# Optimization experiments

Measured on AMD Instinct MI355X. Metric: run time of the kernel, lower is better.

Reference implementation:

```python
import jax, jax.numpy as jnp
import numpy as np

DIM = 1024
HEADS = 8
HEAD_DIM = DIM // HEADS
TAU = HEAD_DIM ** 0.5
BS, SEQ = 1, 2048


def setup_inputs() -> dict:
    key = jax.random.key(0)
    kq, kk, kv, kb = jax.random.split(key, 4)
    q = jax.random.normal(kq, (BS, SEQ, DIM), jnp.float32)
    k = jax.random.normal(kk, (BS, SEQ, DIM), jnp.float32)
    v = jax.random.normal(kv, (BS, SEQ, DIM), jnp.float32)
    Wi_w = jnp.zeros((HEADS, 3 * DIM), jnp.float32)
    Wi_b = 0.1 * jax.random.normal(kb, (HEADS,), jnp.float32)
    Wf_w = jnp.zeros((HEADS, 3 * DIM), jnp.float32)
    Wf_b = jnp.linspace(3.0, 6.0, HEADS, dtype=jnp.float32)  # equidistant_bias_init(3, 6)
    gn_w = jnp.ones((DIM,), jnp.float32)
    gn_b = jnp.zeros((DIM,), jnp.float32)
    return {"q": q, "k": k, "v": v, "Wi_w": Wi_w, "Wi_b": Wi_b,
            "Wf_w": Wf_w, "Wf_b": Wf_b, "gn_w": gn_w, "gn_b": gn_b}


def reference(q, k, v, Wi_w, Wi_b, Wf_w, Wf_b, gn_w, gn_b):
    bs, seq, dim = q.shape
    gate_in = jnp.concatenate([q, k, v], axis=-1)                    # [b, s, 3d]
    itilde = jnp.einsum('bsd,hd->bhs', gate_in, Wi_w) + Wi_b[None, :, None]
    ftilde = jnp.einsum('bsd,hd->bhs', gate_in, Wf_w) + Wf_b[None, :, None]

    # Decay matrix: F_act[i,j] = sum_{t=j+1..i} logsigmoid(ftilde_t), lower-tri else -inf
    csum = jnp.cumsum(jax.nn.log_sigmoid(ftilde), axis=-1)           # [b, h, s]
    Fmat = csum[..., :, None] - csum[..., None, :]                   # [b, h, s, s]
    mask = jnp.tril(jnp.ones((seq, seq), dtype=bool))
    F_act = jnp.where(mask, Fmat, -jnp.inf)

    Dtilde = F_act + itilde[..., None, :]                            # add input gate along j
    max_d = jnp.max(Dtilde, axis=-1, keepdims=True)
    D = jnp.exp(Dtilde - max_d)                                      # stabilized decay weights

    qh = q.reshape(bs, seq, HEADS, HEAD_DIM).transpose(0, 2, 1, 3)
    kh = k.reshape(bs, seq, HEADS, HEAD_DIM).transpose(0, 2, 1, 3)
    vh = v.reshape(bs, seq, HEADS, HEAD_DIM).transpose(0, 2, 1, 3)

    Ctilde = jnp.einsum('bhid,bhjd->bhij', qh, kh) * D / TAU
    maxit = jnp.maximum(jnp.abs(jnp.sum(Ctilde, axis=-1, keepdims=True)), jnp.exp(-max_d))
    Htilde = jnp.einsum('bhij,bhjd->bhid', Ctilde, vh) / (maxit + 1e-6)

    # GroupNorm(HEADS groups) over dim, applied per token
    x = Htilde.transpose(0, 2, 1, 3).reshape(bs * seq, HEADS, HEAD_DIM)
    mean = jnp.mean(x, axis=-1, keepdims=True)
    var = jnp.var(x, axis=-1, keepdims=True)
    xn = (x - mean) / jnp.sqrt(var + 1e-5)
    out = xn.reshape(bs * seq, DIM) * gn_w + gn_b
    return out.reshape(bs, seq, DIM)
```

## Files before the change

### kernel.cpp

```cpp
#include <hip/hip_runtime.h>
#include <math.h>

#define SEQ 2048
#define NH 8
#define HD 128
#define DIMF 1024
#define LOG2E 1.4426950408889634f
#define INVTAU 0.08838834764831845f

typedef __attribute__((ext_vector_type(8))) short bf16x8;
typedef __attribute__((ext_vector_type(8))) unsigned short us8;
typedef __attribute__((ext_vector_type(4))) float f32x4;

__device__ float g_itacc[NH*SEQ];
__device__ float g_ftacc[NH*SEQ];
__device__ float g_aL[NH*SEQ];
__device__ float g_cmL[NH*SEQ];
__device__ float g_en[NH*SEQ];
__device__ unsigned short g_Qb[NH*SEQ*HD];
__device__ unsigned short g_Kb[NH*SEQ*HD];
__device__ unsigned short g_Vb[NH*SEQ*HD];
__device__ unsigned short g_Vt[NH*HD*SEQ];
__device__ unsigned short g_Wb[16*3072];

__device__ __forceinline__ unsigned short f2bf(float x) {
  unsigned u = __float_as_uint(x);
  u += 0x7fffu + ((u >> 16) & 1u);
  return (unsigned short)(u >> 16);
}

__global__ __launch_bounds__(256) void convert_kernel(const float* __restrict__ q,
                                                      const float* __restrict__ k,
                                                      const float* __restrict__ v,
                                                      const float* __restrict__ Wi,
                                                      const float* __restrict__ Wf) {
  const int bid = blockIdx.x;
  if (bid < 6144) {
    const int s = bid & 2047;
    const int t = bid >> 11;
    const float* src = (t == 0) ? q : (t == 1) ? k : v;
    unsigned short* dst = (t == 0) ? g_Qb : (t == 1) ? g_Kb : g_Vb;
    const int c = threadIdx.x * 4;
    const float4 f = *(const float4*)(src + s*DIMF + c);
    const int h = c >> 7, d = c & 127;
    ushort4 u;
    u.x = f2bf(f.x); u.y = f2bf(f.y); u.z = f2bf(f.z); u.w = f2bf(f.w);
    *(ushort4*)(dst + (h*SEQ + s)*HD + d) = u;
  } else {
    const int gid = (bid - 6144) * 256 + threadIdx.x;
    const int e4 = gid * 4;
    const int p = e4 / 3072;
    const int c = e4 % 3072;
    const float* src = (p < 8) ? (Wi + p*3072 + c) : (Wf + (p-8)*3072 + c);
    const float4 f = *(const float4*)src;
    ushort4 u;
    u.x = f2bf(f.x); u.y = f2bf(f.y); u.z = f2bf(f.z); u.w = f2bf(f.w);
    *(ushort4*)(g_Wb + p*3072 + c) = u;
  }
}

__global__ __launch_bounds__(256) void vtrans_kernel() {
  __shared__ __align__(16) unsigned short Ts[64*72];
  const int h  = blockIdx.x;
  const int s0 = blockIdx.y * 64;
  const int d0 = blockIdx.z * 64;
  const int t = threadIdx.x;
  {
    const int sr = t >> 2;
    const int c  = (t & 3) * 16;
    const unsigned short* src = g_Vb + (h*SEQ + s0 + sr)*HD + d0 + c;
    *(us8*)&Ts[sr*72 + c]     = *(const us8*)&src[0];
    *(us8*)&Ts[sr*72 + c + 8] = *(const us8*)&src[8];
  }
  __syncthreads();
  {
    const int w = t >> 6, l = t & 63;
    unsigned short outv[16];
    #pragma unroll
    for (int j = 0; j < 16; ++j) outv[j] = Ts[(w*16 + j)*72 + l];
    unsigned short* dst = g_Vt + (h*HD + d0 + l)*SEQ + s0 + w*16;
    *(us8*)&dst[0] = *(us8*)&outv[0];
    *(us8*)&dst[8] = *(us8*)&outv[8];
  }
}

__global__ __launch_bounds__(256) void gates_kernel() {
  __shared__ f32x4 red[4][64];
  const int tid = threadIdx.x;
  const int wave = tid >> 6, lane = tid & 63;
  const int q4 = lane >> 4, l16 = lane & 15;
  const int s0 = blockIdx.x * 16;
  f32x4 acc = {0.f, 0.f, 0.f, 0.f};
  #pragma unroll 8
  for (int ks = wave*24; ks < wave*24 + 24; ++ks) {
    const int k0 = ks*32 + q4*8;
    const int tsel = k0 >> 10;
    const int rem = k0 & 1023;
    const int hh = rem >> 7, dd = rem & 127;
    const unsigned short* base = (tsel == 0) ? g_Qb : (tsel == 1) ? g_Kb : g_Vb;
    const bf16x8 a = *(const bf16x8*)&base[(hh*SEQ + s0 + l16)*HD + dd];
    const bf16x8 b = *(const bf16x8*)&g_Wb[l16*3072 + k0];
    acc = __builtin_amdgcn_mfma_f32_16x16x32_bf16(a, b, acc, 0, 0, 0);
  }
  red[wave][lane] = acc;
  __syncthreads();
  if (wave == 0) {
    f32x4 s = red[0][lane];
    #pragma unroll
    for (int w = 1; w < 4; ++w) s += red[w][lane];
    #pragma unroll
    for (int r = 0; r < 4; ++r) {
      const int sg = s0 + 4*q4 + r;
      if (l16 < 8) g_itacc[l16*SEQ + sg] = s[r];
      else         g_ftacc[(l16-8)*SEQ + sg] = s[r];
    }
  }
}

__global__ __launch_bounds__(256) void scan_kernel(const float* __restrict__ Wi_b,
                                                   const float* __restrict__ Wf_b) {
  __shared__ float Wsum[4];
  __shared__ float Wmax[4];
  const int h = blockIdx.x;
  const int t = threadIdx.x;
  const int wave = t >> 6, lane = t & 63;
  const float ib = Wi_b[h];
  const float fb = Wf_b[h];
  const int base = h*SEQ + t*8;

  float it[8], ft[8];
  *(float4*)&it[0] = *(const float4*)&g_itacc[base];
  *(float4*)&it[4] = *(const float4*)&g_itacc[base+4];
  *(float4*)&ft[0] = *(const float4*)&g_ftacc[base];
  *(float4*)&ft[4] = *(const float4*)&g_ftacc[base+4];

  float cs[8];
  float run = 0.f;
  #pragma unroll
  for (int j = 0; j < 8; ++j) {
    const float f = ft[j] + fb;
    const float ls = fminf(f, 0.f) - log1pf(expf(-fabsf(f)));
    run += ls;
    cs[j] = run;
  }
  float x = run;
  #pragma unroll
  for (int off = 1; off < 64; off <<= 1) {
    const float tv = __shfl_up(x, off, 64);
    if (lane >= off) x += tv;
  }
  const float wexcl = x - run;
  if (lane == 63) Wsum[wave] = x;
  __syncthreads();
  float boff = 0.f;
  #pragma unroll
  for (int w = 0; w < 4; ++w) if (w < wave) boff += Wsum[w];
  const float cbase = boff + wexcl;

  float a[8], am[8], csum[8];
  float m = -__builtin_inff();
  #pragma unroll
  for (int j = 0; j < 8; ++j) {
    csum[j] = cbase + cs[j];
    a[j] = (it[j] + ib) - csum[j];
    m = fmaxf(m, a[j]);
    am[j] = m;
  }
  float y = m;
  #pragma unroll
  for (int off = 1; off < 64; off <<= 1) {
    const float tv = __shfl_up(y, off, 64);
    if (lane >= off) y = fmaxf(y, tv);
  }
  float e = __shfl_up(y, 1, 64);
  if (lane == 0) e = -__builtin_inff();
  if (lane == 63) Wmax[wave] = y;
  __syncthreads();
  float bmax = -__builtin_inff();
  #pragma unroll
  for (int w = 0; w < 4; ++w) if (w < wave) bmax = fmaxf(bmax, Wmax[w]);
  const float pre = fmaxf(bmax, e);

  float oa[8], ocm[8], oen[8];
  #pragma unroll
  for (int j = 0; j < 8; ++j) {
    const float cm = fmaxf(pre, am[j]);
    oa[j]  = a[j] * LOG2E;
    ocm[j] = cm * LOG2E;
    oen[j] = expf(-(csum[j] + cm));
  }
  *(float4*)&g_aL[base]    = *(float4*)&oa[0];
  *(float4*)&g_aL[base+4]  = *(float4*)&oa[4];
  *(float4*)&g_cmL[base]   = *(float4*)&ocm[0];
  *(float4*)&g_cmL[base+4] = *(float4*)&ocm[4];
  *(float4*)&g_en[base]    = *(float4*)&oen[0];
  *(float4*)&g_en[base+4]  = *(float4*)&oen[4];
}

__global__ __launch_bounds__(256, 2) void attn_kernel(const float* __restrict__ gnw,
                                                      const float* __restrict__ gnb,
                                                      float* __restrict__ out) {
  __shared__ __align__(16) unsigned short Qs[64*136];
  __shared__ __align__(16) unsigned short Ks[64*136];
  __shared__ __align__(16) unsigned short Ps[64*72];
  __shared__ __align__(16) unsigned short Vt[128*72];
  __shared__ float Sred[64][2];
  __shared__ float GNs[64][2][2];

  const int h  = blockIdx.x;
  const int i0 = blockIdx.y * 64;
  const int tid = threadIdx.x;
  const int wave = tid >> 6;
  const int lane = tid & 63;
  const int q4 = lane >> 4;
  const int l16 = lane & 15;
  const int wr = wave >> 1;
  const int wc = wave & 1;

  {
    const unsigned short* Qg = g_Qb + (h*SEQ + i0)*HD;
    const int r0 = tid >> 4;
    const int c8 = (tid & 15) * 8;
    #pragma unroll
    for (int i = 0; i < 4; ++i) {
      const int r = r0 + 16*i;
      *(us8*)&Qs[r*136 + c8] = *(const us8*)&Qg[r*HD + c8];
    }
  }

  float cmv[2][4], env[2][4];
  #pragma unroll
  for (int tr = 0; tr < 2; ++tr)
    #pragma unroll
    for (int r = 0; r < 4; ++r) {
      const int rg = i0 + 32*wr + 16*tr + 4*q4 + r;
      cmv[tr][r] = g_cmL[h*SEQ + rg];
      env[tr][r] = g_en [h*SEQ + rg];
    }

  f32x4 accH[2][4];
  float rs[2][4];
  const f32x4 fzero = {0.f, 0.f, 0.f, 0.f};
  #pragma unroll
  for (int tr = 0; tr < 2; ++tr) {
    #pragma unroll
    for (int tc = 0; tc < 4; ++tc) accH[tr][tc] = fzero;
    #pragma unroll
    for (int r = 0; r < 4; ++r) rs[tr][r] = 0.f;
  }

  for (int j0 = 0; j0 <= i0; j0 += 64) {
    __syncthreads();
    {
      const unsigned short* Kg = g_Kb + (h*SEQ + j0)*HD;
      const int r0 = tid >> 4;
      const int c8 = (tid & 15) * 8;
      #pragma unroll
      for (int i = 0; i < 4; ++i) {
        const int r = r0 + 16*i;
        *(us8*)&Ks[r*136 + c8] = *(const us8*)&Kg[r*HD + c8];
      }
    }
    {
      const unsigned short* Vg = g_Vt + h*HD*SEQ + j0;
      const int d = tid >> 1;
      const int c = (tid & 1) * 32;
      *(us8*)&Vt[d*72 + c]      = *(const us8*)&Vg[d*SEQ + c];
      *(us8*)&Vt[d*72 + c + 8]  = *(const us8*)&Vg[d*SEQ + c + 8];
      *(us8*)&Vt[d*72 + c + 16] = *(const us8*)&Vg[d*SEQ + c + 16];
      *(us8*)&Vt[d*72 + c + 24] = *(const us8*)&Vg[d*SEQ + c + 24];
    }
    float aLv[2];
    aLv[0] = g_aL[h*SEQ + j0 + 32*wc + l16];
    aLv[1] = g_aL[h*SEQ + j0 + 32*wc + 16 + l16];
    __syncthreads();

    f32x4 c00 = fzero, c01 = fzero, c10 = fzero, c11 = fzero;
    #pragma unroll
    for (int ks = 0; ks < 4; ++ks) {
      const int ko = ks*32 + q4*8;
      const bf16x8 a0 = *(const bf16x8*)&Qs[(32*wr      + l16)*136 + ko];
      const bf16x8 a1 = *(const bf16x8*)&Qs[(32*wr + 16 + l16)*136 + ko];
      const bf16x8 b0 = *(const bf16x8*)&Ks[(32*wc      + l16)*136 + ko];
      const bf16x8 b1 = *(const bf16x8*)&Ks[(32*wc + 16 + l16)*136 + ko];
      c00 = __builtin_amdgcn_mfma_f32_16x16x32_bf16(a0, b0, c00, 0, 0, 0);
      c01 = __builtin_amdgcn_mfma_f32_16x16x32_bf16(a0, b1, c01, 0, 0, 0);
      c10 = __builtin_amdgcn_mfma_f32_16x16x32_bf16(a1, b0, c10, 0, 0, 0);
      c11 = __builtin_amdgcn_mfma_f32_16x16x32_bf16(a1, b1, c11, 0, 0, 0);
    }

    const bool diag = (j0 == i0);
    #pragma unroll
    for (int tr = 0; tr < 2; ++tr) {
      #pragma unroll
      for (int tc = 0; tc < 2; ++tc) {
        const f32x4 cc = tr ? (tc ? c11 : c10) : (tc ? c01 : c00);
        const int jg = j0 + 32*wc + 16*tc + l16;
        #pragma unroll
        for (int r = 0; r < 4; ++r) {
          const int rloc = 32*wr + 16*tr + 4*q4 + r;
          const int ig = i0 + rloc;
          const float w = exp2f(aLv[tc] - cmv[tr][r]) * INVTAU;
          float p = cc[r] * w;
          if (diag && (jg > ig)) p = 0.f;
          rs[tr][r] += p;
          Ps[rloc*72 + 32*wc + 16*tc + l16] = f2bf(p);
        }
      }
    }
    __syncthreads();

    #pragma unroll
    for (int ks = 0; ks < 2; ++ks) {
      const int ko = ks*32 + q4*8;
      const bf16x8 p0 = *(const bf16x8*)&Ps[(32*wr      + l16)*72 + ko];
      const bf16x8 p1 = *(const bf16x8*)&Ps[(32*wr + 16 + l16)*72 + ko];
      #pragma unroll
      for (int tc = 0; tc < 4; ++tc) {
        const bf16x8 vb = *(const bf16x8*)&Vt[(64*wc + 16*tc + l16)*72 + ko];
        accH[0][tc] = __builtin_amdgcn_mfma_f32_16x16x32_bf16(p0, vb, accH[0][tc], 0, 0, 0);
        accH[1][tc] = __builtin_amdgcn_mfma_f32_16x16x32_bf16(p1, vb, accH[1][tc], 0, 0, 0);
      }
    }
  }

  #pragma unroll
  for (int tr = 0; tr < 2; ++tr)
    #pragma unroll
    for (int r = 0; r < 4; ++r) {
      float t = rs[tr][r];
      t += __shfl_xor(t, 1, 16);
      t += __shfl_xor(t, 2, 16);
      t += __shfl_xor(t, 4, 16);
      t += __shfl_xor(t, 8, 16);
      rs[tr][r] = t;
    }
  if (l16 == 0) {
    #pragma unroll
    for (int tr = 0; tr < 2; ++tr)
      #pragma unroll
      for (int r = 0; r < 4; ++r)
        Sred[32*wr + 16*tr + 4*q4 + r][wc] = rs[tr][r];
  }
  __syncthreads();

  float gwv[4], gbv[4];
  #pragma unroll
  for (int tc = 0; tc < 4; ++tc) {
    const int dc = 64*wc + 16*tc + l16;
    gwv[tc] = gnw[h*HD + dc];
    gbv[tc] = gnb[h*HD + dc];
  }

  float sx[2][4], sq[2][4];
  #pragma unroll
  for (int tr = 0; tr < 2; ++tr)
    #pragma unroll
    for (int r = 0; r < 4; ++r) {
      const int rloc = 32*wr + 16*tr + 4*q4 + r;
      const float St = Sred[rloc][0] + Sred[rloc][1];
      const float sc = 1.f / (fmaxf(fabsf(St), env[tr][r]) + 1e-6f);
      float s1 = 0.f, s2 = 0.f;
      #pragma unroll
      for (int tc = 0; tc < 4; ++tc) {
        const float xv = accH[tr][tc][r] * sc;
        accH[tr][tc][r] = xv;
        s1 += xv;
        s2 += xv * xv;
      }
      sx[tr][r] = s1;
      sq[tr][r] = s2;
    }
  #pragma unroll
  for (int tr = 0; tr < 2; ++tr)
    #pragma unroll
    for (int r = 0; r < 4; ++r) {
      float a = sx[tr][r], b = sq[tr][r];
      a += __shfl_xor(a, 1, 16); b += __shfl_xor(b, 1, 16);
      a += __shfl_xor(a, 2, 16); b += __shfl_xor(b, 2, 16);
      a += __shfl_xor(a, 4, 16); b += __shfl_xor(b, 4, 16);
      a += __shfl_xor(a, 8, 16); b += __shfl_xor(b, 8, 16);
      sx[tr][r] = a; sq[tr][r] = b;
    }
  if (l16 == 0) {
    #pragma unroll
    for (int tr = 0; tr < 2; ++tr)
      #pragma unroll
      for (int r = 0; r < 4; ++r) {
        const int rloc = 32*wr + 16*tr + 4*q4 + r;
        GNs[rloc][wc][0] = sx[tr][r];
        GNs[rloc][wc][1] = sq[tr][r];
      }
  }
  __syncthreads();

  #pragma unroll
  for (int tr = 0; tr < 2; ++tr)
    #pragma unroll
    for (int r = 0; r < 4; ++r) {
      const int rloc = 32*wr + 16*tr + 4*q4 + r;
      const float s1 = GNs[rloc][0][0] + GNs[rloc][1][0];
      const float s2 = GNs[rloc][0][1] + GNs[rloc][1][1];
      const float mean = s1 * (1.f/128.f);
      const float var  = s2 * (1.f/128.f) - mean*mean;
      const float rstd = rsqrtf(var + 1e-5f);
      float* op = out + (i0 + rloc)*DIMF + h*HD;
      #pragma unroll
      for (int tc = 0; tc < 4; ++tc) {
        const int dc = 64*wc + 16*tc + l16;
        op[dc] = (accH[tr][tc][r] - mean) * rstd * gwv[tc] + gbv[tc];
      }
    }
}

extern "C" void kernel_launch(void* const* d_in, const int* in_sizes, int n_in,
                              void* d_out, int out_size, void* d_ws, size_t ws_size,
                              hipStream_t stream) {
  (void)in_sizes; (void)n_in; (void)out_size; (void)d_ws; (void)ws_size;
  const float* q    = (const float*)d_in[0];
  const float* k    = (const float*)d_in[1];
  const float* v    = (const float*)d_in[2];
  const float* Wi_w = (const float*)d_in[3];
  const float* Wi_b = (const float*)d_in[4];
  const float* Wf_w = (const float*)d_in[5];
  const float* Wf_b = (const float*)d_in[6];
  const float* gnw  = (const float*)d_in[7];
  const float* gnb  = (const float*)d_in[8];
  float* out = (float*)d_out;

  convert_kernel<<<dim3(6192), 256, 0, stream>>>(q, k, v, Wi_w, Wf_w);
  vtrans_kernel<<<dim3(NH, SEQ/64, HD/64), 256, 0, stream>>>();
  gates_kernel<<<dim3(128), 256, 0, stream>>>();
  scan_kernel<<<dim3(NH), 256, 0, stream>>>(Wi_b, Wf_b);
  attn_kernel<<<dim3(NH, SEQ/64), 256, 0, stream>>>(gnw, gnb, out);
}
```

Measured before the change: 171.4 us.

## Split causal attention along the key axis into balanced chunks with a separate reduce

```diff
diff --git a/kernel.cpp b/kernel.cpp
--- a/kernel.cpp
+++ b/kernel.cpp
@@ -22,6 +22,8 @@
 __device__ unsigned short g_Vb[NH*SEQ*HD];
 __device__ unsigned short g_Vt[NH*HD*SEQ];
 __device__ unsigned short g_Wb[16*3072];
+__device__ float g_Opart[640*64*128];
+__device__ float g_Spart[640*64];
 
 __device__ __forceinline__ unsigned short f2bf(float x) {
   unsigned u = __float_as_uint(x);
@@ -197,18 +199,27 @@
   *(float4*)&g_en[base+4]  = *(float4*)&oen[4];
 }
 
-__global__ __launch_bounds__(256, 2) void attn_kernel(const float* __restrict__ gnw,
-                                                      const float* __restrict__ gnb,
-                                                      float* __restrict__ out) {
-  __shared__ __align__(16) unsigned short Qs[64*136];
+__global__ __launch_bounds__(256, 2) void attn1_kernel() {
   __shared__ __align__(16) unsigned short Ks[64*136];
   __shared__ __align__(16) unsigned short Ps[64*72];
   __shared__ __align__(16) unsigned short Vt[128*72];
   __shared__ float Sred[64][2];
-  __shared__ float GNs[64][2][2];
-
-  const int h  = blockIdx.x;
-  const int i0 = blockIdx.y * 64;
+
+  const int h = blockIdx.x;
+  const int y = blockIdx.y;
+  int g, s0g;
+  if      (y < 8)  { g = 0; s0g = 0;  }
+  else if (y < 24) { g = 1; s0g = 8;  }
+  else if (y < 48) { g = 2; s0g = 24; }
+  else             { g = 3; s0g = 48; }
+  const int rel = y - s0g;
+  const int iT  = 8*g + rel/(g+1);
+  const int ch  = rel - (rel/(g+1))*(g+1);
+  const int slot = h*80 + y;
+  const int i0 = iT*64;
+  const int jt0 = ch*8;
+  const int jt1 = (jt0 + 8 < iT + 1) ? (jt0 + 8) : (iT + 1);
+
   const int tid = threadIdx.x;
   const int wave = tid >> 6;
   const int lane = tid & 63;
@@ -217,26 +228,22 @@
   const int wr = wave >> 1;
   const int wc = wave & 1;
 
+  bf16x8 qa[2][4];
   {
-    const unsigned short* Qg = g_Qb + (h*SEQ + i0)*HD;
-    const int r0 = tid >> 4;
-    const int c8 = (tid & 15) * 8;
-    #pragma unroll
-    for (int i = 0; i < 4; ++i) {
-      const int r = r0 + 16*i;
-      *(us8*)&Qs[r*136 + c8] = *(const us8*)&Qg[r*HD + c8];
-    }
-  }
-
-  float cmv[2][4], env[2][4];
+    const unsigned short* Qg = g_Qb + (h*SEQ + i0 + 32*wr + l16)*HD;
+    #pragma unroll
+    for (int tr = 0; tr < 2; ++tr)
+      #pragma unroll
+      for (int ks = 0; ks < 4; ++ks)
+        qa[tr][ks] = *(const bf16x8*)&Qg[tr*16*HD + ks*32 + q4*8];
+  }
+
+  float cmv[2][4];
   #pragma unroll
   for (int tr = 0; tr < 2; ++tr)
     #pragma unroll
-    for (int r = 0; r < 4; ++r) {
-      const int rg = i0 + 32*wr + 16*tr + 4*q4 + r;
-      cmv[tr][r] = g_cmL[h*SEQ + rg];
-      env[tr][r] = g_en [h*SEQ + rg];
-    }
+    for (int r = 0; r < 4; ++r)
+      cmv[tr][r] = g_cmL[h*SEQ + i0 + 32*wr + 16*tr + 4*q4 + r];
 
   f32x4 accH[2][4];
   float rs[2][4];
@@ -249,47 +256,58 @@
     for (int r = 0; r < 4; ++r) rs[tr][r] = 0.f;
   }
 
-  for (int j0 = 0; j0 <= i0; j0 += 64) {
+  const int r0 = tid >> 4;
+  const int c8 = (tid & 15) * 8;
+  const int dK = tid >> 1;
+  const int cV = (tid & 1) * 32;
+
+  const unsigned short* Kgh = g_Kb + h*SEQ*HD;
+  const unsigned short* Vgh = g_Vt + h*HD*SEQ;
+
+  us8 Kr[4], Vr[4];
+  {
+    const unsigned short* kp = Kgh + jt0*64*HD;
+    const unsigned short* vp = Vgh + jt0*64;
+    #pragma unroll
+    for (int i = 0; i < 4; ++i) Kr[i] = *(const us8*)&kp[(r0 + 16*i)*HD + c8];
+    #pragma unroll
+    for (int j = 0; j < 4; ++j) Vr[j] = *(const us8*)&vp[dK*SEQ + cV + 8*j];
+  }
+
+  for (int jt = jt0; jt < jt1; ++jt) {
+    const int j0 = jt*64;
     __syncthreads();
-    {
-      const unsigned short* Kg = g_Kb + (h*SEQ + j0)*HD;
-      const int r0 = tid >> 4;
-      const int c8 = (tid & 15) * 8;
-      #pragma unroll
-      for (int i = 0; i < 4; ++i) {
-        const int r = r0 + 16*i;
-        *(us8*)&Ks[r*136 + c8] = *(const us8*)&Kg[r*HD + c8];
-      }
-    }
-    {
-      const unsigned short* Vg = g_Vt + h*HD*SEQ + j0;
-      const int d = tid >> 1;
-      const int c = (tid & 1) * 32;
-      *(us8*)&Vt[d*72 + c]      = *(const us8*)&Vg[d*SEQ + c];
-      *(us8*)&Vt[d*72 + c + 8]  = *(const us8*)&Vg[d*SEQ + c + 8];
-      *(us8*)&Vt[d*72 + c + 16] = *(const us8*)&Vg[d*SEQ + c + 16];
-      *(us8*)&Vt[d*72 + c + 24] = *(const us8*)&Vg[d*SEQ + c + 24];
-    }
+    #pragma unroll
+    for (int i = 0; i < 4; ++i) *(us8*)&Ks[(r0 + 16*i)*136 + c8] = Kr[i];
+    #pragma unroll
+    for (int j = 0; j < 4; ++j) *(us8*)&Vt[dK*72 + cV + 8*j] = Vr[j];
     float aLv[2];
     aLv[0] = g_aL[h*SEQ + j0 + 32*wc + l16];
     aLv[1] = g_aL[h*SEQ + j0 + 32*wc + 16 + l16];
     __syncthreads();
 
+    if (jt + 1 < jt1) {
+      const unsigned short* kp = Kgh + (j0 + 64)*HD;
+      const unsigned short* vp = Vgh + (j0 + 64);
+      #pragma unroll
+      for (int i = 0; i < 4; ++i) Kr[i] = *(const us8*)&kp[(r0 + 16*i)*HD + c8];
+      #pragma unroll
+      for (int j = 0; j < 4; ++j) Vr[j] = *(const us8*)&vp[dK*SEQ + cV + 8*j];
+    }
+
     f32x4 c00 = fzero, c01 = fzero, c10 = fzero, c11 = fzero;
     #pragma unroll
     for (int ks = 0; ks < 4; ++ks) {
       const int ko = ks*32 + q4*8;
-      const bf16x8 a0 = *(const bf16x8*)&Qs[(32*wr      + l16)*136 + ko];
-      const bf16x8 a1 = *(const bf16x8*)&Qs[(32*wr + 16 + l16)*136 + ko];
       const bf16x8 b0 = *(const bf16x8*)&Ks[(32*wc      + l16)*136 + ko];
       const bf16x8 b1 = *(const bf16x8*)&Ks[(32*wc + 16 + l16)*136 + ko];
-      c00 = __builtin_amdgcn_mfma_f32_16x16x32_bf16(a0, b0, c00, 0, 0, 0);
-      c01 = __builtin_amdgcn_mfma_f32_16x16x32_bf16(a0, b1, c01, 0, 0, 0);
-      c10 = __builtin_amdgcn_mfma_f32_16x16x32_bf16(a1, b0, c10, 0, 0, 0);
-      c11 = __builtin_amdgcn_mfma_f32_16x16x32_bf16(a1, b1, c11, 0, 0, 0);
-    }
-
-    const bool diag = (j0 == i0);
+      c00 = __builtin_amdgcn_mfma_f32_16x16x32_bf16(qa[0][ks], b0, c00, 0, 0, 0);
+      c01 = __builtin_amdgcn_mfma_f32_16x16x32_bf16(qa[0][ks], b1, c01, 0, 0, 0);
+      c10 = __builtin_amdgcn_mfma_f32_16x16x32_bf16(qa[1][ks], b0, c10, 0, 0, 0);
+      c11 = __builtin_amdgcn_mfma_f32_16x16x32_bf16(qa[1][ks], b1, c11, 0, 0, 0);
+    }
+
+    const bool diag = (jt == iT);
     #pragma unroll
     for (int tr = 0; tr < 2; ++tr) {
       #pragma unroll
@@ -344,73 +362,76 @@
   }
   __syncthreads();
 
-  float gwv[4], gbv[4];
-  #pragma unroll
-  for (int tc = 0; tc < 4; ++tc) {
-    const int dc = 64*wc + 16*tc + l16;
-    gwv[tc] = gnw[h*HD + dc];
-    gbv[tc] = gnb[h*HD + dc];
-  }
-
-  float sx[2][4], sq[2][4];
+  if (tid < 64) g_Spart[slot*64 + tid] = Sred[tid][0] + Sred[tid][1];
+
+  float* Ob = g_Opart + slot*(64*128);
   #pragma unroll
   for (int tr = 0; tr < 2; ++tr)
     #pragma unroll
     for (int r = 0; r < 4; ++r) {
       const int rloc = 32*wr + 16*tr + 4*q4 + r;
-      const float St = Sred[rloc][0] + Sred[rloc][1];
-      const float sc = 1.f / (fmaxf(fabsf(St), env[tr][r]) + 1e-6f);
-      float s1 = 0.f, s2 = 0.f;
-      #pragma unroll
-      for (int tc = 0; tc < 4; ++tc) {
-        const float xv = accH[tr][tc][r] * sc;
-        accH[tr][tc][r] = xv;
-        s1 += xv;
-        s2 += xv * xv;
-      }
-      sx[tr][r] = s1;
-      sq[tr][r] = s2;
-    }
-  #pragma unroll
-  for (int tr = 0; tr < 2; ++tr)
-    #pragma unroll
-    for (int r = 0; r < 4; ++r) {
-      float a = sx[tr][r], b = sq[tr][r];
-      a += __shfl_xor(a, 1, 16); b += __shfl_xor(b, 1, 16);
-      a += __shfl_xor(a, 2, 16); b += __shfl_xor(b, 2, 16);
-      a += __shfl_xor(a, 4, 16); b += __shfl_xor(b, 4, 16);
-      a += __shfl_xor(a, 8, 16); b += __shfl_xor(b, 8, 16);
-      sx[tr][r] = a; sq[tr][r] = b;
-    }
-  if (l16 == 0) {
-    #pragma unroll
-    for (int tr = 0; tr < 2; ++tr)
-      #pragma unroll
-      for (int r = 0; r < 4; ++r) {
-        const int rloc = 32*wr + 16*tr + 4*q4 + r;
-        GNs[rloc][wc][0] = sx[tr][r];
-        GNs[rloc][wc][1] = sq[tr][r];
-      }
-  }
-  __syncthreads();
-
-  #pragma unroll
-  for (int tr = 0; tr < 2; ++tr)
-    #pragma unroll
-    for (int r = 0; r < 4; ++r) {
-      const int rloc = 32*wr + 16*tr + 4*q4 + r;
-      const float s1 = GNs[rloc][0][0] + GNs[rloc][1][0];
-      const float s2 = GNs[rloc][0][1] + GNs[rloc][1][1];
-      const float mean = s1 * (1.f/128.f);
-      const float var  = s2 * (1.f/128.f) - mean*mean;
-      const float rstd = rsqrtf(var + 1e-5f);
-      float* op = out + (i0 + rloc)*DIMF + h*HD;
-      #pragma unroll
-      for (int tc = 0; tc < 4; ++tc) {
-        const int dc = 64*wc + 16*tc + l16;
-        op[dc] = (accH[tr][tc][r] - mean) * rstd * gwv[tc] + gbv[tc];
-      }
-    }
+      #pragma unroll
+      for (int tc = 0; tc < 4; ++tc)
+        Ob[rloc*128 + 64*wc + 16*tc + l16] = accH[tr][tc][r];
+    }
+}
+
+__global__ __launch_bounds__(256) void reduce_kernel(const float* __restrict__ gnw,
+                                                     const float* __restrict__ gnb,
+                                                     float* __restrict__ out) {
+  const int h  = blockIdx.x;
+  const int iT = blockIdx.y;
+  const int t  = threadIdx.x;
+  const int r  = t >> 2;
+  const int qd = t & 3;
+  const int qq = iT >> 3;
+  const int nch = qq + 1;
+  const int slot0 = h*80 + iT + 4*qq*(qq-1) + qq*(iT & 7);
+
+  float acc[32];
+  #pragma unroll
+  for (int e = 0; e < 32; ++e) acc[e] = 0.f;
+  float S = 0.f;
+  for (int c = 0; c < nch; ++c) {
+    const float* Ob = g_Opart + (slot0 + c)*(64*128) + r*128 + qd*32;
+    #pragma unroll
+    for (int kk = 0; kk < 8; ++kk) {
+      const float4 f = *(const float4*)&Ob[kk*4];
+      acc[kk*4+0] += f.x; acc[kk*4+1] += f.y; acc[kk*4+2] += f.z; acc[kk*4+3] += f.w;
+    }
+    S += g_Spart[(slot0 + c)*64 + r];
+  }
+
+  const float en = g_en[h*SEQ + iT*64 + r];
+  const float sc = 1.f / (fmaxf(fabsf(S), en) + 1e-6f);
+  float s1 = 0.f, s2 = 0.f;
+  #pragma unroll
+  for (int e = 0; e < 32; ++e) {
+    const float xv = acc[e] * sc;
+    acc[e] = xv;
+    s1 += xv;
+    s2 += xv * xv;
+  }
+  s1 += __shfl_xor(s1, 1, 4); s2 += __shfl_xor(s2, 1, 4);
+  s1 += __shfl_xor(s1, 2, 4); s2 += __shfl_xor(s2, 2, 4);
+  const float mean = s1 * (1.f/128.f);
+  const float var  = s2 * (1.f/128.f) - mean*mean;
+  const float rstd = rsqrtf(var + 1e-5f);
+
+  const float* gw = gnw + h*HD + qd*32;
+  const float* gb = gnb + h*HD + qd*32;
+  float* op = out + (iT*64 + r)*DIMF + h*HD + qd*32;
+  #pragma unroll
+  for (int kk = 0; kk < 8; ++kk) {
+    const float4 w4 = *(const float4*)&gw[kk*4];
+    const float4 b4 = *(const float4*)&gb[kk*4];
+    float4 o;
+    o.x = (acc[kk*4+0] - mean) * rstd * w4.x + b4.x;
+    o.y = (acc[kk*4+1] - mean) * rstd * w4.y + b4.y;
+    o.z = (acc[kk*4+2] - mean) * rstd * w4.z + b4.z;
+    o.w = (acc[kk*4+3] - mean) * rstd * w4.w + b4.w;
+    *(float4*)&op[kk*4] = o;
+  }
 }
 
 extern "C" void kernel_launch(void* const* d_in, const int* in_sizes, int n_in,
@@ -432,5 +453,6 @@
   vtrans_kernel<<<dim3(NH, SEQ/64, HD/64), 256, 0, stream>>>();
   gates_kernel<<<dim3(128), 256, 0, stream>>>();
   scan_kernel<<<dim3(NH), 256, 0, stream>>>(Wi_b, Wf_b);
-  attn_kernel<<<dim3(NH, SEQ/64), 256, 0, stream>>>(gnw, gnb, out);
-}
+  attn1_kernel<<<dim3(NH, 80), 256, 0, stream>>>();
+  reduce_kernel<<<dim3(NH, SEQ/64), 256, 0, stream>>>(gnw, gnb, out);
+}
```

Measured after the change: 159.1 us. 1.08x faster.
